# Performance work log

Hardware: AMD Instinct MI355X
Metric: run time of the kernel (lower is better)

Reference implementation:

```python
import jax, jax.numpy as jnp
import numpy as np

HID = 2048
NH = 16
HD = HID // NH
FF = 8192
SEQ = 2048
B = 1
EPS = 1e-05
ROPE_BASE = 10000.0


def _layernorm(x, w, b):
    mu = jnp.mean(x, axis=-1, keepdims=True)
    var = jnp.mean(jnp.square(x - mu), axis=-1, keepdims=True)
    return (x - mu) * jax.lax.rsqrt(var + EPS) * w + b


def _rope(x, offset):
    # x: [B, S, H, D]; rotate-half LLaMA-style rotary embedding
    S, D = x.shape[1], x.shape[3]
    inv_freq = 1.0 / (ROPE_BASE ** (jnp.arange(0, D, 2, dtype=jnp.float32) / D))  # [D/2]
    pos = jnp.arange(S, dtype=jnp.float32) + offset
    ang = pos[:, None] * inv_freq[None, :]                     # [S, D/2]
    cos = jnp.cos(ang)[None, :, None, :]                       # [1,S,1,D/2]
    sin = jnp.sin(ang)[None, :, None, :]
    x1, x2 = x[..., : D // 2], x[..., D // 2 :]
    return jnp.concatenate([x1 * cos - x2 * sin, x2 * cos + x1 * sin], axis=-1)


def setup_inputs() -> dict:
    key = jax.random.key(0)
    ks = jax.random.split(key, 16)
    sd = 0.02
    inp = {
        "hidden_states": jax.random.normal(ks[0], (B, SEQ, HID), dtype=jnp.float32),
        # additive causal mask as fed to multi_head_attention_forward
        "attention_mask": jnp.where(
            jnp.tril(jnp.ones((SEQ, SEQ), dtype=bool)), 0.0, -1e9
        ).astype(jnp.float32),
        "ln1_w": jnp.ones((HID,), jnp.float32),
        "ln1_b": jnp.zeros((HID,), jnp.float32),
        "ln2_w": jnp.ones((HID,), jnp.float32),
        "ln2_b": jnp.zeros((HID,), jnp.float32),
        "wq": jax.random.normal(ks[1], (HID, HID), jnp.float32) * sd,
        "bq": jnp.zeros((HID,), jnp.float32),
        "wk": jax.random.normal(ks[2], (HID, HID), jnp.float32) * sd,
        "bk": jnp.zeros((HID,), jnp.float32),
        "wv": jax.random.normal(ks[3], (HID, HID), jnp.float32) * sd,
        "bv": jnp.zeros((HID,), jnp.float32),
        "wo": jax.random.normal(ks[4], (HID, HID), jnp.float32) * sd,
        "bo": jnp.zeros((HID,), jnp.float32),
        "w_gate": jax.random.normal(ks[5], (FF, HID), jnp.float32) * sd,
        "w_up": jax.random.normal(ks[6], (FF, HID), jnp.float32) * sd,
        "w_down": jax.random.normal(ks[7], (HID, FF), jnp.float32) * sd,
        "total_seq_len": SEQ,
    }
    return inp


def reference(hidden_states, attention_mask, ln1_w, ln1_b, ln2_w, ln2_b,
              wq, bq, wk, bk, wv, bv, wo, bo, w_gate, w_up, w_down,
              total_seq_len):
    Bv, S, _ = hidden_states.shape
    x = _layernorm(hidden_states, ln1_w, ln1_b)
    q = (x @ wq.T + bq).reshape(Bv, S, NH, HD)
    k = (x @ wk.T + bk).reshape(Bv, S, NH, HD)
    v = (x @ wv.T + bv).reshape(Bv, S, NH, HD)
    offset = total_seq_len - S  # 0 for prefill
    q = _rope(q, offset)
    k = _rope(k, offset)
    # cache of max_sequence_length zeros concatenated with k/v then sliced to the
    # last total_seq_len entries == just the current k/v when total_seq_len == S
    scale = 1.0 / np.sqrt(HD)
    scores = jnp.einsum("bshd,bthd->bhst", q, k) * scale + attention_mask[None, None]
    probs = jax.nn.softmax(scores, axis=-1)
    attn = jnp.einsum("bhst,bthd->bshd", probs, v).reshape(Bv, S, HID)
    attn = attn @ wo.T + bo
    h = hidden_states + attn
    y = _layernorm(h, ln2_w, ln2_b)
    ffn = (jax.nn.silu(y @ w_gate.T) * (y @ w_up.T)) @ w_down.T
    return h + ffn
```

## Files before the change

### kernel.cpp

```cpp
#include <hip/hip_runtime.h>

#define HIDN 2048
#define NHEAD 16
#define HDIM 128
#define FFDIM 8192
#define SEQLEN 2048

typedef __attribute__((ext_vector_type(8))) __bf16 bf16x8;
typedef __attribute__((ext_vector_type(4))) float f32x4;
typedef __attribute__((ext_vector_type(4))) unsigned short u16x4;
typedef __attribute__((ext_vector_type(8))) unsigned short u16x8;

__device__ __forceinline__ unsigned short f2bfu(float f) {
    unsigned int u = __float_as_uint(f);
    unsigned int r = u + 0x7fffu + ((u >> 16) & 1u);
    return (unsigned short)(r >> 16);
}
__device__ __forceinline__ float bfu2f(unsigned short u) {
    return __uint_as_float(((unsigned int)u) << 16);
}

__device__ __forceinline__ void gload16(const void* g, void* l) {
    __builtin_amdgcn_global_load_lds(
        (const __attribute__((address_space(1))) unsigned int*)g,
        (__attribute__((address_space(3))) unsigned int*)l,
        16, 0, 0);
}

__device__ __forceinline__ void conv_groups(const float* __restrict__ src,
                                            unsigned short* __restrict__ dst,
                                            int i0, int stride, int n8) {
    for (int i = i0; i < n8; i += stride) {
        float4 a = ((const float4*)src)[i * 2];
        float4 b = ((const float4*)src)[i * 2 + 1];
        u16x8 v;
        v[0] = f2bfu(a.x); v[1] = f2bfu(a.y); v[2] = f2bfu(a.z); v[3] = f2bfu(a.w);
        v[4] = f2bfu(b.x); v[5] = f2bfu(b.y); v[6] = f2bfu(b.z); v[7] = f2bfu(b.w);
        *(u16x8*)(dst + (size_t)i * 8) = v;
    }
}

__device__ __forceinline__ void conv_tail3(const float* __restrict__ s0,
                                           const float* __restrict__ s1,
                                           const float* __restrict__ s2,
                                           unsigned short* __restrict__ dst,
                                           int i0, int stride, int nmat) {
    const int FF8 = FFDIM * HIDN / 8;
    const int tot = nmat * FF8;
    for (int i = i0; i < tot; i += stride) {
        int m = i >> 21;
        int li = i & (FF8 - 1);
        const float* s = (m == 0) ? s0 : (m == 1) ? s1 : s2;
        float4 a = ((const float4*)s)[li * 2];
        float4 b = ((const float4*)s)[li * 2 + 1];
        u16x8 v;
        v[0] = f2bfu(a.x); v[1] = f2bfu(a.y); v[2] = f2bfu(a.z); v[3] = f2bfu(a.w);
        v[4] = f2bfu(b.x); v[5] = f2bfu(b.y); v[6] = f2bfu(b.z); v[7] = f2bfu(b.w);
        *(u16x8*)(dst + (size_t)i * 8) = v;
    }
}

__global__ __launch_bounds__(256)
void conv_f32_bf16(const float* __restrict__ src, unsigned short* __restrict__ dst) {
    int i = blockIdx.x * 256 + threadIdx.x;
    conv_groups(src, dst, i, 1 << 30, i + 1);
}

__global__ __launch_bounds__(256)
void conv3_f32_bf16(const float* __restrict__ s0, const float* __restrict__ s1,
                    const float* __restrict__ s2, unsigned short* __restrict__ dst) {
    int i = blockIdx.x * 256 + threadIdx.x;
    int m = i >> 19;
    int li = i & ((1 << 19) - 1);
    const float* s = (m == 0) ? s0 : (m == 1) ? s1 : s2;
    float4 a = ((const float4*)s)[li * 2];
    float4 b = ((const float4*)s)[li * 2 + 1];
    u16x8 v;
    v[0] = f2bfu(a.x); v[1] = f2bfu(a.y); v[2] = f2bfu(a.z); v[3] = f2bfu(a.w);
    v[4] = f2bfu(b.x); v[5] = f2bfu(b.y); v[6] = f2bfu(b.z); v[7] = f2bfu(b.w);
    *(u16x8*)(dst + (size_t)i * 8) = v;
}

__global__ __launch_bounds__(256)
void ln_bf16(const float* __restrict__ x, const float* __restrict__ w,
             const float* __restrict__ b, unsigned short* __restrict__ out) {
    const int row = blockIdx.x;
    const int tid = threadIdx.x;
    const float* xr = x + (size_t)row * HIDN;
    float4 v0 = ((const float4*)xr)[tid];
    float4 v1 = ((const float4*)xr)[tid + 256];
    float s = v0.x + v0.y + v0.z + v0.w + v1.x + v1.y + v1.z + v1.w;
    float q = v0.x*v0.x + v0.y*v0.y + v0.z*v0.z + v0.w*v0.w
            + v1.x*v1.x + v1.y*v1.y + v1.z*v1.z + v1.w*v1.w;
    for (int o = 32; o > 0; o >>= 1) {
        s += __shfl_down(s, o, 64);
        q += __shfl_down(q, o, 64);
    }
    __shared__ float red[8];
    const int wid = tid >> 6;
    if ((tid & 63) == 0) { red[wid] = s; red[4 + wid] = q; }
    __syncthreads();
    float st = red[0] + red[1] + red[2] + red[3];
    float qt = red[4] + red[5] + red[6] + red[7];
    float mu = st * (1.0f / HIDN);
    float var = qt * (1.0f / HIDN) - mu * mu;
    float rs = rsqrtf(var + 1e-5f);
    unsigned short* orow = out + (size_t)row * HIDN;
    int i0 = tid * 4, i1 = (tid + 256) * 4;
    orow[i0 + 0] = f2bfu((v0.x - mu) * rs * w[i0 + 0] + b[i0 + 0]);
    orow[i0 + 1] = f2bfu((v0.y - mu) * rs * w[i0 + 1] + b[i0 + 1]);
    orow[i0 + 2] = f2bfu((v0.z - mu) * rs * w[i0 + 2] + b[i0 + 2]);
    orow[i0 + 3] = f2bfu((v0.w - mu) * rs * w[i0 + 3] + b[i0 + 3]);
    orow[i1 + 0] = f2bfu((v1.x - mu) * rs * w[i1 + 0] + b[i1 + 0]);
    orow[i1 + 1] = f2bfu((v1.y - mu) * rs * w[i1 + 1] + b[i1 + 1]);
    orow[i1 + 2] = f2bfu((v1.z - mu) * rs * w[i1 + 2] + b[i1 + 2]);
    orow[i1 + 3] = f2bfu((v1.w - mu) * rs * w[i1 + 3] + b[i1 + 3]);
}

__global__ __launch_bounds__(256)
void wo_ln(const unsigned short* __restrict__ part, const float* __restrict__ h,
           const float* __restrict__ bo, const float* __restrict__ w,
           const float* __restrict__ b, float* __restrict__ out,
           unsigned short* __restrict__ ybf) {
    const int row = blockIdx.x;
    const int tid = threadIdx.x;
    const int c0 = tid * 4, c1 = (tid + 256) * 4;
    float4 o0 = ((const float4*)(h + (size_t)row * HIDN))[tid];
    float4 o1 = ((const float4*)(h + (size_t)row * HIDN))[tid + 256];
    o0.x += bo[c0]; o0.y += bo[c0 + 1]; o0.z += bo[c0 + 2]; o0.w += bo[c0 + 3];
    o1.x += bo[c1]; o1.y += bo[c1 + 1]; o1.z += bo[c1 + 2]; o1.w += bo[c1 + 3];
#pragma unroll
    for (int sk = 0; sk < 4; ++sk) {
        const unsigned short* pr = part + (size_t)sk * 4194304 + (size_t)row * HIDN;
        u16x4 p0 = *(const u16x4*)(pr + c0);
        u16x4 p1 = *(const u16x4*)(pr + c1);
        o0.x += bfu2f(p0[0]); o0.y += bfu2f(p0[1]); o0.z += bfu2f(p0[2]); o0.w += bfu2f(p0[3]);
        o1.x += bfu2f(p1[0]); o1.y += bfu2f(p1[1]); o1.z += bfu2f(p1[2]); o1.w += bfu2f(p1[3]);
    }
    ((float4*)(out + (size_t)row * HIDN))[tid] = o0;
    ((float4*)(out + (size_t)row * HIDN))[tid + 256] = o1;
    float s = o0.x + o0.y + o0.z + o0.w + o1.x + o1.y + o1.z + o1.w;
    float q = o0.x*o0.x + o0.y*o0.y + o0.z*o0.z + o0.w*o0.w
            + o1.x*o1.x + o1.y*o1.y + o1.z*o1.z + o1.w*o1.w;
    for (int o = 32; o > 0; o >>= 1) {
        s += __shfl_down(s, o, 64);
        q += __shfl_down(q, o, 64);
    }
    __shared__ float red[8];
    const int wid = tid >> 6;
    if ((tid & 63) == 0) { red[wid] = s; red[4 + wid] = q; }
    __syncthreads();
    float st = red[0] + red[1] + red[2] + red[3];
    float qt = red[4] + red[5] + red[6] + red[7];
    float mu = st * (1.0f / HIDN);
    float var = qt * (1.0f / HIDN) - mu * mu;
    float rs = rsqrtf(var + 1e-5f);
    unsigned short* yr = ybf + (size_t)row * HIDN;
    yr[c0 + 0] = f2bfu((o0.x - mu) * rs * w[c0 + 0] + b[c0 + 0]);
    yr[c0 + 1] = f2bfu((o0.y - mu) * rs * w[c0 + 1] + b[c0 + 1]);
    yr[c0 + 2] = f2bfu((o0.z - mu) * rs * w[c0 + 2] + b[c0 + 2]);
    yr[c0 + 3] = f2bfu((o0.w - mu) * rs * w[c0 + 3] + b[c0 + 3]);
    yr[c1 + 0] = f2bfu((o1.x - mu) * rs * w[c1 + 0] + b[c1 + 0]);
    yr[c1 + 1] = f2bfu((o1.y - mu) * rs * w[c1 + 1] + b[c1 + 1]);
    yr[c1 + 2] = f2bfu((o1.z - mu) * rs * w[c1 + 2] + b[c1 + 2]);
    yr[c1 + 3] = f2bfu((o1.w - mu) * rs * w[c1 + 3] + b[c1 + 3]);
}

__global__ __launch_bounds__(256)
void rope_kernel(unsigned short* __restrict__ qk, const int* __restrict__ tsl) {
    int id = blockIdx.x * 256 + threadIdx.x;
    int p  = id & 63;
    int hh = (id >> 6) & 31;
    int s  = id >> 11;
    int off = tsl[0] - SEQLEN;
    float inv = exp2f((float)p * -0.20762050593f);
    float ang = (float)(s + off) * inv;
    float c, sn;
    __sincosf(ang, &sn, &c);
    size_t base = (size_t)s * 4096 + hh * 128 + p;
    float x1 = bfu2f(qk[base]);
    float x2 = bfu2f(qk[base + 64]);
    qk[base]      = f2bfu(x1 * c - x2 * sn);
    qk[base + 64] = f2bfu(x2 * c + x1 * sn);
}

#define BAR __builtin_amdgcn_s_barrier()
#define VM4 asm volatile("s_waitcnt vmcnt(4)" ::: "memory")
#define VM0 asm volatile("s_waitcnt vmcnt(0)" ::: "memory")

#define STAGE_A(tile, h) { const int k0_ = k_start + (tile) * 64;                      \
  _Pragma("unroll") for (int i_ = 0; i_ < 2; ++i_) {                                   \
    int d_ = (h) * 16384 + i_ * 8192 + tid * 16;                                       \
    int r_ = d_ >> 7;                                                                  \
    int cb_ = (d_ & 127) ^ ((r_ & 7) << 4);                                            \
    gload16((const char*)Ab + ((size_t)(brow + r_) * lda + k0_) * 2 + cb_,             \
            smem + ((tile) & 1) * 65536 + (h) * 16384 + i_ * 8192 + w * 1024); } }

#define STAGE_B(tile, h) { const int k0_ = k_start + (tile) * 64;                      \
  _Pragma("unroll") for (int i_ = 0; i_ < 2; ++i_) {                                   \
    int d_ = (h) * 16384 + i_ * 8192 + tid * 16;                                       \
    int r_ = d_ >> 7;                                                                  \
    int cb_ = (d_ & 127) ^ ((r_ & 7) << 4);                                            \
    gload16((const char*)Bb + ((size_t)(bcol + r_) * ldb + k0_) * 2 + cb_,             \
            smem + ((tile) & 1) * 65536 + 32768 + (h) * 16384 + i_ * 8192 + w * 1024); } }

#define LDB(BO)                                                                        \
  _Pragma("unroll") for (int n_ = 0; n_ < 4; ++n_)                                     \
  _Pragma("unroll") for (int kk_ = 0; kk_ < 2; ++kk_)                                  \
    bF[n_][kk_] = *(const bf16x8*)(smem + (BO) + bbase + n_ * 2048 + colb[kk_]);

#define LDA2(BO, MP)                                                                   \
  _Pragma("unroll") for (int dm_ = 0; dm_ < 2; ++dm_)                                  \
  _Pragma("unroll") for (int kk_ = 0; kk_ < 2; ++kk_)                                  \
    aF[dm_][kk_] = *(const bf16x8*)(smem + (BO) + abase + ((MP) * 2 + dm_) * 2048 + colb[kk_]);

#define MM(MP)                                                                         \
  __builtin_amdgcn_s_setprio(1);                                                       \
  _Pragma("unroll") for (int dm_ = 0; dm_ < 2; ++dm_)                                  \
  _Pragma("unroll") for (int n_ = 0; n_ < 4; ++n_)                                     \
  _Pragma("unroll") for (int kk_ = 0; kk_ < 2; ++kk_)                                  \
    acc[(MP) * 2 + dm_][n_] = __builtin_amdgcn_mfma_f32_16x16x32_bf16(                 \
        aF[dm_][kk_], bF[n_][kk_], acc[(MP) * 2 + dm_][n_], 0, 0, 0);                  \
  __builtin_amdgcn_s_setprio(0);

template<int EPI>
__global__ __launch_bounds__(512, 1)
void gemm256(const unsigned short* __restrict__ Ab, int lda,
             const unsigned short* __restrict__ Bb, int ldb,
             int k_len, int nbx, int ldc,
             const float* __restrict__ bias0, const float* __restrict__ bias1,
             const float* __restrict__ bias2,
             unsigned short* __restrict__ outB, unsigned short* __restrict__ outV,
             int ngemm, const float* __restrict__ csrc,
             unsigned short* __restrict__ cdst, int conv_n8) {
    extern __shared__ char smem[];
    const int tid = threadIdx.x;

    if ((int)blockIdx.x >= ngemm) {
        if (blockIdx.y == 0) {
            const int nconv = gridDim.x - ngemm;
            conv_groups(csrc, cdst, (blockIdx.x - ngemm) * 512 + tid, nconv * 512, conv_n8);
        }
        return;
    }

    const int w = tid >> 6, lane = tid & 63;
    const int lr = lane & 15, lg = lane >> 4;
    const int wrow = (w >> 2) * 128;
    const int wc = w & 3;

    const int cpx = nbx >> 3;
    const int xcd = blockIdx.x & 7;
    const int loc = blockIdx.x >> 3;
    const int bx = xcd * cpx + loc % cpx;
    const int by = loc / cpx;
    const int brow = by * 256, bcol = bx * 256;
    const int k_start = blockIdx.y * k_len;

    const int xorv = (lr & 7) << 4;
    int colb[2];
    colb[0] = (lg * 16) ^ xorv;
    colb[1] = (64 + lg * 16) ^ xorv;
    const int abase = (wrow + lr) * 128;
    const int bbase = 32768 + (wc * 64 + lr) * 128;

    f32x4 acc[8][4];
#pragma unroll
    for (int m = 0; m < 8; ++m)
#pragma unroll
        for (int n = 0; n < 4; ++n) acc[m][n] = (f32x4){0.f, 0.f, 0.f, 0.f};

    bf16x8 bF[4][2], aF[2][2];

    const int NT = k_len >> 6;
    const int NIT = NT >> 1;

    STAGE_A(0, 0); STAGE_A(0, 1); STAGE_B(0, 0); STAGE_B(0, 1);
    STAGE_B(1, 0); STAGE_B(1, 1);
    VM4; BAR;

    for (int it = 0; it < NIT; ++it) {
        const int T = 2 * it;
        const bool s2 = (T + 2) < NT, s3 = (T + 3) < NT;
        LDB(0); LDA2(0, 0); STAGE_A(T + 1, 0); MM(0); BAR;
        LDA2(0, 1); STAGE_A(T + 1, 1); MM(1); BAR;
        LDA2(0, 2); if (s2) STAGE_B(T + 2, 0); MM(2); BAR;
        LDA2(0, 3); if (s2) STAGE_B(T + 2, 1); MM(3);
        if (s2) { VM4; } else { VM0; }
        BAR;
        LDB(65536); LDA2(65536, 0); if (s2) STAGE_A(T + 2, 0); MM(0); BAR;
        LDA2(65536, 1); if (s2) STAGE_A(T + 2, 1); MM(1); BAR;
        LDA2(65536, 2); if (s3) STAGE_B(T + 3, 0); MM(2); BAR;
        LDA2(65536, 3); if (s3) STAGE_B(T + 3, 1); MM(3);
        if (s3) { VM4; } else { VM0; }
        BAR;
    }

    char* sw = smem + w * 16384;
    const bool vblk = (EPI == 0) && (bcol >= 4096);

    if (!vblk) {
#pragma unroll
        for (int n = 0; n < 4; ++n) {
            const int col = bcol + wc * 64 + n * 16 + lr;
            float bv = 0.f;
            if (EPI == 0) bv = (col < 2048) ? bias0[col] : bias1[col - 2048];
#pragma unroll
            for (int m = 0; m < 8; ++m)
#pragma unroll
                for (int j = 0; j < 4; ++j) {
                    const int r = m * 16 + lg * 4 + j;
                    const int cb = ((n * 16 + lr) * 2) ^ ((r & 7) << 4);
                    *(unsigned short*)(sw + r * 128 + cb) = f2bfu(acc[m][n][j] + bv);
                }
        }
        const int rl = lane >> 3, cl = lane & 7;
#pragma unroll
        for (int it2 = 0; it2 < 16; ++it2) {
            const int r = it2 * 8 + rl;
            const int cb = (cl * 16) ^ ((r & 7) << 4);
            u16x8 val = *(const u16x8*)(sw + r * 128 + cb);
            const int gr = brow + wrow + r;
            const int gcol = bcol + wc * 64 + cl * 8;
            if (EPI == 0) {
                *(u16x8*)(outB + (size_t)gr * 4096 + gcol) = val;
            } else if (EPI == 1) {
                *(u16x8*)(outB + (size_t)gr * ldc + gcol) = val;
            } else if (EPI == 3) {
                unsigned short* gp = outB + (size_t)gr * ldc + gcol;
                u16x8 gv = *(const u16x8*)gp;
                u16x8 ov;
#pragma unroll
                for (int e = 0; e < 8; ++e) {
                    float g = bfu2f(gv[e]);
                    float uu = bfu2f(val[e]);
                    ov[e] = f2bfu(g / (1.0f + __expf(-g)) * uu);
                }
                *(u16x8*)gp = ov;
            } else {
                *(u16x8*)(outB + (size_t)blockIdx.y * 4194304 + (size_t)gr * ldc + gcol) = val;
            }
        }
    } else {
#pragma unroll
        for (int n = 0; n < 4; ++n) {
            const int c = n * 16 + lr;
            const float bv = bias2[bcol - 4096 + wc * 64 + c];
            const int cx = (c & 7) << 4;
#pragma unroll
            for (int m = 0; m < 8; ++m) {
                const int r0 = m * 16 + lg * 4;
                u16x4 pk;
#pragma unroll
                for (int j = 0; j < 4; ++j) pk[j] = f2bfu(acc[m][n][j] + bv);
                *(u16x4*)(sw + c * 256 + ((r0 * 2) ^ cx)) = pk;
            }
        }
        const int cg = lane >> 4, rl2 = lane & 15;
#pragma unroll
        for (int it2 = 0; it2 < 16; ++it2) {
            const int c = it2 * 4 + cg;
            const int rb = (rl2 * 16) ^ ((c & 7) << 4);
            u16x8 val = *(const u16x8*)(sw + c * 256 + rb);
            const int d = bcol - 4096 + wc * 64 + c;
            *(u16x8*)(outV + (size_t)d * SEQLEN + brow + wrow + rl2 * 8) = val;
        }
    }
}

__global__ __launch_bounds__(256)
void reduce4_add(const unsigned short* __restrict__ part, float* __restrict__ out) {
    int i = blockIdx.x * 256 + threadIdx.x;
    float4 o = ((const float4*)out)[i];
#pragma unroll
    for (int sk = 0; sk < 4; ++sk) {
        u16x4 p = ((const u16x4*)(part + (size_t)sk * 4194304))[i];
        o.x += bfu2f(p[0]); o.y += bfu2f(p[1]); o.z += bfu2f(p[2]); o.w += bfu2f(p[3]);
    }
    ((float4*)out)[i] = o;
}

#define PST 72
__global__ __launch_bounds__(256)
void attn_kernel(const unsigned short* __restrict__ QK, const unsigned short* __restrict__ VT,
                 unsigned short* __restrict__ O,
                 const float* __restrict__ c0, const float* __restrict__ c1,
                 const float* __restrict__ c2, unsigned short* __restrict__ cdst,
                 int nmat) {
    __shared__ __align__(16) unsigned short Ks[2][64 * 128];
    __shared__ __align__(16) unsigned short Vs[2][128 * 64];
    __shared__ __align__(16) unsigned short Ps[4][16 * PST];
    const int tid = threadIdx.x;

    if ((int)blockIdx.x >= 256) {
        const int nconv = gridDim.x - 256;
        conv_tail3(c0, c1, c2, cdst, (blockIdx.x - 256) * 256 + tid, nconv * 256, nmat);
        return;
    }

    const int lane = tid & 63;
    const int w = tid >> 6;
    const int lr = lane & 15, lg = lane >> 4;

    const int id = blockIdx.x;
    const int h = ((id & 7) << 1) | ((id >> 3) & 1);
    const int p = id >> 4;

    const unsigned short* Kb = QK + 2048 + h * 128;
    const unsigned short* Vb = VT + (size_t)(h * 128) * SEQLEN;

    int krow[4], kcb[4], vrow[4], vcb[4];
#pragma unroll
    for (int ch = 0; ch < 4; ++ch) {
        int d = ch * 4096 + w * 1024 + lane * 16;
        krow[ch] = d >> 8;
        kcb[ch]  = (d & 255) ^ ((krow[ch] & 7) << 4);
        vrow[ch] = d >> 7;
        vcb[ch]  = (d & 127) ^ ((vrow[ch] & 7) << 4);
    }

    const float sc2 = 0.08838834764831845f * 1.44269504089f;
    bf16x8 ones;
#pragma unroll
    for (int e = 0; e < 8; ++e) ones[e] = (__bf16)1.0f;

#pragma unroll 1
    for (int seg = 0; seg < 2; ++seg) {
        const int qb = seg ? (31 - p) : p;
        const int qw = qb * 64 + w * 16;
        const unsigned short* Qb = QK + (size_t)qw * 4096 + h * 128;

        bf16x8 qa[4];
#pragma unroll
        for (int c = 0; c < 4; ++c)
            qa[c] = *(const bf16x8*)(Qb + (size_t)lr * 4096 + c * 32 + lg * 8);

        f32x4 acc[8];
#pragma unroll
        for (int dt = 0; dt < 8; ++dt) acc[dt] = (f32x4){0.f, 0.f, 0.f, 0.f};
        f32x4 lacc = (f32x4){0.f, 0.f, 0.f, 0.f};
        const int ntile = qb + 1;

#pragma unroll
        for (int ch = 0; ch < 4; ++ch) {
            gload16(Kb + (size_t)krow[ch] * 4096 + (kcb[ch] >> 1),
                    (char*)&Ks[0][0] + ch * 4096 + w * 1024);
            gload16(Vb + (size_t)vrow[ch] * SEQLEN + (vcb[ch] >> 1),
                    (char*)&Vs[0][0] + ch * 4096 + w * 1024);
        }
        __syncthreads();

        for (int tt = 0; tt < ntile; ++tt) {
            const int cur = tt & 1;
            const int t0 = tt * 64;
            if (tt + 1 < ntile) {
                const int t1 = t0 + 64;
#pragma unroll
                for (int ch = 0; ch < 4; ++ch) {
                    gload16(Kb + (size_t)(t1 + krow[ch]) * 4096 + (kcb[ch] >> 1),
                            (char*)&Ks[cur ^ 1][0] + ch * 4096 + w * 1024);
                    gload16(Vb + (size_t)vrow[ch] * SEQLEN + t1 + (vcb[ch] >> 1),
                            (char*)&Vs[cur ^ 1][0] + ch * 4096 + w * 1024);
                }
            }
            f32x4 s[4];
#pragma unroll
            for (int th = 0; th < 4; ++th) s[th] = (f32x4){0.f, 0.f, 0.f, 0.f};
            __builtin_amdgcn_s_setprio(1);
#pragma unroll
            for (int th = 0; th < 4; ++th) {
                const int row = th * 16 + lr;
#pragma unroll
                for (int c = 0; c < 4; ++c) {
                    bf16x8 kb = *(const bf16x8*)((char*)&Ks[cur][0] + row * 256 +
                                                 ((c * 64 + lg * 16) ^ ((lr & 7) << 4)));
                    s[th] = __builtin_amdgcn_mfma_f32_16x16x32_bf16(qa[c], kb, s[th], 0, 0, 0);
                }
            }
            __builtin_amdgcn_s_setprio(0);
            if (tt == qb) {
#pragma unroll
                for (int th = 0; th < 4; ++th) {
                    int tg = t0 + th * 16 + lr;
#pragma unroll
                    for (int jj = 0; jj < 4; ++jj) {
                        int qg = qw + lg * 4 + jj;
                        float v = s[th][jj] * sc2 + (tg <= qg ? 0.f : -1e9f);
                        s[th][jj] = exp2f(v);
                    }
                }
            } else {
#pragma unroll
                for (int th = 0; th < 4; ++th)
#pragma unroll
                    for (int jj = 0; jj < 4; ++jj)
                        s[th][jj] = exp2f(s[th][jj] * sc2);
            }
#pragma unroll
            for (int th = 0; th < 4; ++th)
#pragma unroll
                for (int jj = 0; jj < 4; ++jj)
                    Ps[w][(lg * 4 + jj) * PST + th * 16 + lr] = f2bfu(s[th][jj]);
            bf16x8 pa[2];
#pragma unroll
            for (int ks = 0; ks < 2; ++ks)
                pa[ks] = *(const bf16x8*)&Ps[w][lr * PST + ks * 32 + lg * 8];
            __builtin_amdgcn_s_setprio(1);
            lacc = __builtin_amdgcn_mfma_f32_16x16x32_bf16(pa[0], ones, lacc, 0, 0, 0);
            lacc = __builtin_amdgcn_mfma_f32_16x16x32_bf16(pa[1], ones, lacc, 0, 0, 0);
#pragma unroll
            for (int dt = 0; dt < 8; ++dt) {
                const int d = dt * 16 + lr;
#pragma unroll
                for (int ks = 0; ks < 2; ++ks) {
                    bf16x8 vb = *(const bf16x8*)((char*)&Vs[cur][0] + d * 128 +
                                                 ((ks * 64 + lg * 16) ^ ((lr & 7) << 4)));
                    acc[dt] = __builtin_amdgcn_mfma_f32_16x16x32_bf16(pa[ks], vb, acc[dt], 0, 0, 0);
                }
            }
            __builtin_amdgcn_s_setprio(0);
            __syncthreads();
        }
        float invl[4];
#pragma unroll
        for (int jj = 0; jj < 4; ++jj) invl[jj] = 1.0f / lacc[jj];
#pragma unroll
        for (int dt = 0; dt < 8; ++dt)
#pragma unroll
            for (int jj = 0; jj < 4; ++jj)
                O[(size_t)(qw + lg * 4 + jj) * HIDN + h * HDIM + dt * 16 + lr] =
                    f2bfu(acc[dt][jj] * invl[jj]);
    }
}

extern "C" void kernel_launch(void* const* d_in, const int* in_sizes, int n_in,
                              void* d_out, int out_size, void* d_ws, size_t ws_size,
                              hipStream_t stream) {
    const float* hidden = (const float*)d_in[0];
    const float* ln1w = (const float*)d_in[2];
    const float* ln1b = (const float*)d_in[3];
    const float* ln2w = (const float*)d_in[4];
    const float* ln2b = (const float*)d_in[5];
    const float* wq = (const float*)d_in[6];
    const float* bq = (const float*)d_in[7];
    const float* wk = (const float*)d_in[8];
    const float* bk = (const float*)d_in[9];
    const float* wv = (const float*)d_in[10];
    const float* bv = (const float*)d_in[11];
    const float* wo = (const float*)d_in[12];
    const float* bo = (const float*)d_in[13];
    const float* wg = (const float*)d_in[14];
    const float* wu = (const float*)d_in[15];
    const float* wd = (const float*)d_in[16];
    const int* tsl = (const int*)d_in[17];
    float* out = (float*)d_out;

    char* ws = (char*)d_ws;
    const size_t MB = 1024 * 1024;
    unsigned short* Wbuf = (unsigned short*)(ws);
    unsigned short* qk   = (unsigned short*)(ws + 32 * MB);
    unsigned short* vt   = (unsigned short*)(ws + 48 * MB);
    unsigned short* x_bf = (unsigned short*)(ws + 56 * MB);
    unsigned short* g_bf = (unsigned short*)(ws + 64 * MB);
    unsigned short* part = qk;
    unsigned short* y_bf = vt;

    const int HID2 = HIDN * HIDN;
    const int FFE  = FFDIM * HIDN;
    const int CONV_HID = HID2 / 8 / 256;
    const int CONV_FF  = FFE / 8 / 256;
    const size_t LDSZ = 131072;

    int nmat = 0;
    if (ws_size >= 192 * MB) nmat = 3;
    else if (ws_size >= 160 * MB) nmat = 2;
    else if (ws_size >= 128 * MB) nmat = 1;
    unsigned short* wgBuf = (nmat > 0) ? (unsigned short*)(ws + 96 * MB) : Wbuf;
    unsigned short* wuBuf = (nmat > 1) ? wgBuf + (size_t)FFE : Wbuf;
    unsigned short* wdBuf = (nmat > 2) ? wgBuf + 2 * (size_t)FFE : Wbuf;

    conv3_f32_bf16<<<3 * CONV_HID, 256, 0, stream>>>(wq, wk, wv, Wbuf);
    ln_bf16<<<SEQLEN, 256, 0, stream>>>(hidden, ln1w, ln1b, x_bf);
    gemm256<0><<<dim3(192 + 64, 1), 512, LDSZ, stream>>>(
        x_bf, HIDN, Wbuf, HIDN, HIDN, 24, 0, bq, bk, bv, qk, vt,
        192, wo, Wbuf + 3 * (size_t)HID2, HID2 / 8);
    rope_kernel<<<SEQLEN * 32 * 64 / 256, 256, 0, stream>>>(qk, tsl);

    if (nmat > 0) {
        attn_kernel<<<768, 256, 0, stream>>>(qk, vt, x_bf, wg, wu, wd, wgBuf, nmat);
    } else {
        attn_kernel<<<256, 256, 0, stream>>>(qk, vt, x_bf, nullptr, nullptr, nullptr,
                                             nullptr, 0);
    }

    gemm256<4><<<dim3(64, 4), 512, LDSZ, stream>>>(
        x_bf, HIDN, Wbuf + 3 * (size_t)HID2, HIDN, 512, 8, HIDN,
        nullptr, nullptr, nullptr, g_bf, nullptr, 64, nullptr, nullptr, 0);
    wo_ln<<<SEQLEN, 256, 0, stream>>>(g_bf, hidden, bo, ln2w, ln2b, out, y_bf);

    if (nmat < 1) conv_f32_bf16<<<CONV_FF, 256, 0, stream>>>(wg, Wbuf);
    gemm256<1><<<dim3(256, 1), 512, LDSZ, stream>>>(
        y_bf, HIDN, wgBuf, HIDN, HIDN, 32, FFDIM,
        nullptr, nullptr, nullptr, g_bf, nullptr, 256, nullptr, nullptr, 0);
    if (nmat < 2) conv_f32_bf16<<<CONV_FF, 256, 0, stream>>>(wu, Wbuf);
    gemm256<3><<<dim3(256, 1), 512, LDSZ, stream>>>(
        y_bf, HIDN, wuBuf, HIDN, HIDN, 32, FFDIM,
        nullptr, nullptr, nullptr, g_bf, nullptr, 256, nullptr, nullptr, 0);
    if (nmat < 3) conv_f32_bf16<<<CONV_FF, 256, 0, stream>>>(wd, Wbuf);
    gemm256<4><<<dim3(64, 4), 512, LDSZ, stream>>>(
        g_bf, FFDIM, wdBuf, FFDIM, 2048, 8, HIDN,
        nullptr, nullptr, nullptr, part, nullptr, 64, nullptr, nullptr, 0);
    reduce4_add<<<4096, 256, 0, stream>>>(part, out);
}
```

Measured before the change: 406.4 us.

## Add 128x256 single-buffered GEMM for FFN and Wo, specialize QKV kernel

Introduces a new gemm128 kernel with a 128x256 block tile, a simple single-stage load/compute loop and 48KB LDS, and uses it for the Wo, gate, up and down projections with twice as many blocks. The previous 256x256 kernel with its deep double-buffered pipeline is kept only for the QKV projection and de-templated. The aim is more blocks per GPU and potentially multiple blocks per CU, giving better occupancy and wave balance. The cost is less data reuse per block and no in-kernel load/compute overlap, since the new kernel waits on each tile before computing.

```diff
diff --git a/kernel.cpp b/kernel.cpp
--- a/kernel.cpp
+++ b/kernel.cpp
@@ -223,24 +223,21 @@
         aF[dm_][kk_], bF[n_][kk_], acc[(MP) * 2 + dm_][n_], 0, 0, 0);                  \
   __builtin_amdgcn_s_setprio(0);
 
-template<int EPI>
 __global__ __launch_bounds__(512, 1)
-void gemm256(const unsigned short* __restrict__ Ab, int lda,
-             const unsigned short* __restrict__ Bb, int ldb,
-             int k_len, int nbx, int ldc,
-             const float* __restrict__ bias0, const float* __restrict__ bias1,
-             const float* __restrict__ bias2,
-             unsigned short* __restrict__ outB, unsigned short* __restrict__ outV,
-             int ngemm, const float* __restrict__ csrc,
-             unsigned short* __restrict__ cdst, int conv_n8) {
+void gemm256_qkv(const unsigned short* __restrict__ Ab, int lda,
+                 const unsigned short* __restrict__ Bb, int ldb,
+                 int k_len, int nbx,
+                 const float* __restrict__ bias0, const float* __restrict__ bias1,
+                 const float* __restrict__ bias2,
+                 unsigned short* __restrict__ outB, unsigned short* __restrict__ outV,
+                 int ngemm, const float* __restrict__ csrc,
+                 unsigned short* __restrict__ cdst, int conv_n8) {
     extern __shared__ char smem[];
     const int tid = threadIdx.x;
 
     if ((int)blockIdx.x >= ngemm) {
-        if (blockIdx.y == 0) {
-            const int nconv = gridDim.x - ngemm;
-            conv_groups(csrc, cdst, (blockIdx.x - ngemm) * 512 + tid, nconv * 512, conv_n8);
-        }
+        conv_groups(csrc, cdst, (blockIdx.x - ngemm) * 512 + tid,
+                    (gridDim.x - ngemm) * 512, conv_n8);
         return;
     }
 
@@ -255,7 +252,7 @@
     const int bx = xcd * cpx + loc % cpx;
     const int by = loc / cpx;
     const int brow = by * 256, bcol = bx * 256;
-    const int k_start = blockIdx.y * k_len;
+    const int k_start = 0;
 
     const int xorv = (lr & 7) << 4;
     int colb[2];
@@ -297,14 +294,13 @@
     }
 
     char* sw = smem + w * 16384;
-    const bool vblk = (EPI == 0) && (bcol >= 4096);
+    const bool vblk = bcol >= 4096;
 
     if (!vblk) {
 #pragma unroll
         for (int n = 0; n < 4; ++n) {
             const int col = bcol + wc * 64 + n * 16 + lr;
-            float bv = 0.f;
-            if (EPI == 0) bv = (col < 2048) ? bias0[col] : bias1[col - 2048];
+            float bv = (col < 2048) ? bias0[col] : bias1[col - 2048];
 #pragma unroll
             for (int m = 0; m < 8; ++m)
 #pragma unroll
@@ -320,26 +316,7 @@
             const int r = it2 * 8 + rl;
             const int cb = (cl * 16) ^ ((r & 7) << 4);
             u16x8 val = *(const u16x8*)(sw + r * 128 + cb);
-            const int gr = brow + wrow + r;
-            const int gcol = bcol + wc * 64 + cl * 8;
-            if (EPI == 0) {
-                *(u16x8*)(outB + (size_t)gr * 4096 + gcol) = val;
-            } else if (EPI == 1) {
-                *(u16x8*)(outB + (size_t)gr * ldc + gcol) = val;
-            } else if (EPI == 3) {
-                unsigned short* gp = outB + (size_t)gr * ldc + gcol;
-                u16x8 gv = *(const u16x8*)gp;
-                u16x8 ov;
-#pragma unroll
-                for (int e = 0; e < 8; ++e) {
-                    float g = bfu2f(gv[e]);
-                    float uu = bfu2f(val[e]);
-                    ov[e] = f2bfu(g / (1.0f + __expf(-g)) * uu);
-                }
-                *(u16x8*)gp = ov;
-            } else {
-                *(u16x8*)(outB + (size_t)blockIdx.y * 4194304 + (size_t)gr * ldc + gcol) = val;
-            }
+            *(u16x8*)(outB + (size_t)(brow + wrow + r) * 4096 + bcol + wc * 64 + cl * 8) = val;
         }
     } else {
 #pragma unroll
@@ -364,6 +341,136 @@
             u16x8 val = *(const u16x8*)(sw + c * 256 + rb);
             const int d = bcol - 4096 + wc * 64 + c;
             *(u16x8*)(outV + (size_t)d * SEQLEN + brow + wrow + rl2 * 8) = val;
+        }
+    }
+}
+
+#define STG128 { const int k0_ = k_start + T1 * 64;                                    \
+  _Pragma("unroll") for (int i_ = 0; i_ < 2; ++i_) {                                   \
+    int d_ = i_ * 8192 + tid * 16;                                                     \
+    int r_ = d_ >> 7;                                                                  \
+    int cb_ = (d_ & 127) ^ ((r_ & 7) << 4);                                            \
+    gload16((const char*)Ab + ((size_t)(brow + r_) * lda + k0_) * 2 + cb_,             \
+            smem + i_ * 8192 + w * 1024); }                                            \
+  _Pragma("unroll") for (int i_ = 0; i_ < 4; ++i_) {                                   \
+    int d_ = i_ * 8192 + tid * 16;                                                     \
+    int r_ = d_ >> 7;                                                                  \
+    int cb_ = (d_ & 127) ^ ((r_ & 7) << 4);                                            \
+    gload16((const char*)Bb + ((size_t)(bcol + r_) * ldb + k0_) * 2 + cb_,             \
+            smem + 16384 + i_ * 8192 + w * 1024); } }
+
+template<int EPI>
+__global__ __launch_bounds__(512)
+void gemm128(const unsigned short* __restrict__ Ab, int lda,
+             const unsigned short* __restrict__ Bb, int ldb,
+             int k_len, int nbx, int ldc,
+             unsigned short* __restrict__ outB) {
+    extern __shared__ char smem[];
+    const int tid = threadIdx.x;
+    const int w = tid >> 6, lane = tid & 63;
+    const int lr = lane & 15, lg = lane >> 4;
+    const int wrow = (w >> 2) * 64;
+    const int wc = w & 3;
+
+    const int cpx = nbx >> 3;
+    const int xcd = blockIdx.x & 7;
+    const int loc = blockIdx.x >> 3;
+    const int bx = xcd * cpx + loc % cpx;
+    const int by = loc / cpx;
+    const int brow = by * 128, bcol = bx * 256;
+    const int k_start = blockIdx.y * k_len;
+
+    const int xorv = (lr & 7) << 4;
+    int colb[2];
+    colb[0] = (lg * 16) ^ xorv;
+    colb[1] = (64 + lg * 16) ^ xorv;
+    const int abase = (wrow + lr) * 128;
+    const int bbase = 16384 + (wc * 64 + lr) * 128;
+
+    f32x4 acc[4][4];
+#pragma unroll
+    for (int m = 0; m < 4; ++m)
+#pragma unroll
+        for (int n = 0; n < 4; ++n) acc[m][n] = (f32x4){0.f, 0.f, 0.f, 0.f};
+
+    bf16x8 bF[4][2], aF[4][2];
+
+    const int NT = k_len >> 6;
+
+    { const int T1 = 0; STG128; }
+    for (int T = 0; T < NT; ++T) {
+        VM0; BAR;
+#pragma unroll
+        for (int n = 0; n < 4; ++n)
+#pragma unroll
+            for (int kk = 0; kk < 2; ++kk)
+                bF[n][kk] = *(const bf16x8*)(smem + bbase + n * 2048 + colb[kk]);
+#pragma unroll
+        for (int m = 0; m < 4; ++m)
+#pragma unroll
+            for (int kk = 0; kk < 2; ++kk)
+                aF[m][kk] = *(const bf16x8*)(smem + abase + m * 2048 + colb[kk]);
+        __builtin_amdgcn_s_setprio(1);
+#pragma unroll
+        for (int m = 0; m < 4; ++m)
+#pragma unroll
+            for (int n = 0; n < 4; ++n)
+#pragma unroll
+                for (int kk = 0; kk < 2; ++kk)
+                    acc[m][n] = __builtin_amdgcn_mfma_f32_16x16x32_bf16(
+                        aF[m][kk], bF[n][kk], acc[m][n], 0, 0, 0);
+        __builtin_amdgcn_s_setprio(0);
+        __syncthreads();
+        if (T + 1 < NT) { const int T1 = T + 1; STG128; }
+    }
+
+    const int w4 = w & 3;
+    const int pass = w >> 2;
+    char* sw = smem + w4 * 8192;
+    const int rl = lane >> 3, cl = lane & 7;
+
+#pragma unroll
+    for (int p = 0; p < 2; ++p) {
+        __syncthreads();
+        if (pass == p) {
+#pragma unroll
+            for (int n = 0; n < 4; ++n)
+#pragma unroll
+                for (int m = 0; m < 4; ++m)
+#pragma unroll
+                    for (int j = 0; j < 4; ++j) {
+                        const int r = m * 16 + lg * 4 + j;
+                        const int cb = ((n * 16 + lr) * 2) ^ ((r & 7) << 4);
+                        *(unsigned short*)(sw + r * 128 + cb) = f2bfu(acc[m][n][j]);
+                    }
+        }
+        __syncthreads();
+        if (pass == p) {
+#pragma unroll
+            for (int it2 = 0; it2 < 8; ++it2) {
+                const int r = it2 * 8 + rl;
+                const int cb = (cl * 16) ^ ((r & 7) << 4);
+                u16x8 val = *(const u16x8*)(sw + r * 128 + cb);
+                const int gr = brow + wrow + r;
+                const int gcol = bcol + wc * 64 + cl * 8;
+                if (EPI == 1) {
+                    *(u16x8*)(outB + (size_t)gr * ldc + gcol) = val;
+                } else if (EPI == 3) {
+                    unsigned short* gp = outB + (size_t)gr * ldc + gcol;
+                    u16x8 gv = *(const u16x8*)gp;
+                    u16x8 ov;
+#pragma unroll
+                    for (int e = 0; e < 8; ++e) {
+                        float g = bfu2f(gv[e]);
+                        float uu = bfu2f(val[e]);
+                        ov[e] = f2bfu(g / (1.0f + __expf(-g)) * uu);
+                    }
+                    *(u16x8*)gp = ov;
+                } else {
+                    *(u16x8*)(outB + (size_t)blockIdx.y * 4194304 +
+                              (size_t)gr * ldc + gcol) = val;
+                }
+            }
         }
     }
 }
@@ -570,6 +677,7 @@
     const int CONV_HID = HID2 / 8 / 256;
     const int CONV_FF  = FFE / 8 / 256;
     const size_t LDSZ = 131072;
+    const size_t LDSZ128 = 49152;
 
     int nmat = 0;
     if (ws_size >= 192 * MB) nmat = 3;
@@ -581,8 +689,8 @@
 
     conv3_f32_bf16<<<3 * CONV_HID, 256, 0, stream>>>(wq, wk, wv, Wbuf);
     ln_bf16<<<SEQLEN, 256, 0, stream>>>(hidden, ln1w, ln1b, x_bf);
-    gemm256<0><<<dim3(192 + 64, 1), 512, LDSZ, stream>>>(
-        x_bf, HIDN, Wbuf, HIDN, HIDN, 24, 0, bq, bk, bv, qk, vt,
+    gemm256_qkv<<<256, 512, LDSZ, stream>>>(
+        x_bf, HIDN, Wbuf, HIDN, HIDN, 24, bq, bk, bv, qk, vt,
         192, wo, Wbuf + 3 * (size_t)HID2, HID2 / 8);
     rope_kernel<<<SEQLEN * 32 * 64 / 256, 256, 0, stream>>>(qk, tsl);
 
@@ -593,22 +701,18 @@
                                              nullptr, 0);
     }
 
-    gemm256<4><<<dim3(64, 4), 512, LDSZ, stream>>>(
-        x_bf, HIDN, Wbuf + 3 * (size_t)HID2, HIDN, 512, 8, HIDN,
-        nullptr, nullptr, nullptr, g_bf, nullptr, 64, nullptr, nullptr, 0);
+    gemm128<4><<<dim3(128, 4), 512, LDSZ128, stream>>>(
+        x_bf, HIDN, Wbuf + 3 * (size_t)HID2, HIDN, 512, 8, HIDN, g_bf);
     wo_ln<<<SEQLEN, 256, 0, stream>>>(g_bf, hidden, bo, ln2w, ln2b, out, y_bf);
 
     if (nmat < 1) conv_f32_bf16<<<CONV_FF, 256, 0, stream>>>(wg, Wbuf);
-    gemm256<1><<<dim3(256, 1), 512, LDSZ, stream>>>(
-        y_bf, HIDN, wgBuf, HIDN, HIDN, 32, FFDIM,
-        nullptr, nullptr, nullptr, g_bf, nullptr, 256, nullptr, nullptr, 0);
+    gemm128<1><<<dim3(512, 1), 512, LDSZ128, stream>>>(
+        y_bf, HIDN, wgBuf, HIDN, HIDN, 32, FFDIM, g_bf);
     if (nmat < 2) conv_f32_bf16<<<CONV_FF, 256, 0, stream>>>(wu, Wbuf);
-    gemm256<3><<<dim3(256, 1), 512, LDSZ, stream>>>(
-        y_bf, HIDN, wuBuf, HIDN, HIDN, 32, FFDIM,
-        nullptr, nullptr, nullptr, g_bf, nullptr, 256, nullptr, nullptr, 0);
+    gemm128<3><<<dim3(512, 1), 512, LDSZ128, stream>>>(
+        y_bf, HIDN, wuBuf, HIDN, HIDN, 32, FFDIM, g_bf);
     if (nmat < 3) conv_f32_bf16<<<CONV_FF, 256, 0, stream>>>(wd, Wbuf);
-    gemm256<4><<<dim3(64, 4), 512, LDSZ, stream>>>(
-        g_bf, FFDIM, wdBuf, FFDIM, 2048, 8, HIDN,
-        nullptr, nullptr, nullptr, part, nullptr, 64, nullptr, nullptr, 0);
+    gemm128<4><<<dim3(128, 4), 512, LDSZ128, stream>>>(
+        g_bf, FFDIM, wdBuf, FFDIM, 2048, 8, HIDN, part);
     reduce4_add<<<4096, 256, 0, stream>>>(part, out);
 }
```

Result: slower. 573.8 us (+41.2%).
